# Kernel optimization log

Hardware: AMD Instinct MI355X
Metric: run time of the kernel (lower is better)

The kernel has to match this reference:

```python
import jax, jax.numpy as jnp
import numpy as np

H, KV, D, HID = 32, 8, 128, 4096  # heads, kv heads, head_dim, hidden
BLOCK = 64
SEQLENS = [512, 768, 512, 256]  # packed continuous batch, T = 2048
NUM_BLOCKS = 64


def setup_inputs() -> dict:
    key = jax.random.key(0)
    ks = jax.random.split(key, 8)
    T = int(sum(SEQLENS))
    position_ids = jnp.asarray(np.concatenate([np.arange(l) for l in SEQLENS]), jnp.int64 if False else jnp.int32)
    seq_ids = jnp.asarray(np.concatenate([np.full(l, b) for b, l in enumerate(SEQLENS)]), jnp.int32)
    # assign cache blocks sequentially per sequence, pad rows with 0 (never read)
    max_blocks = max((l + BLOCK - 1) // BLOCK for l in SEQLENS)
    bo = np.zeros((len(SEQLENS), max_blocks), np.int32)
    nxt = 0
    for b, l in enumerate(SEQLENS):
        nb = (l + BLOCK - 1) // BLOCK
        bo[b, :nb] = np.arange(nxt, nxt + nb)
        nxt += nb
    block_offsets = jnp.asarray(bo)
    vision_mask = jax.random.uniform(ks[0], (T,)) < 0.3
    s = 0.02
    return {
        'hidden_states': jax.random.normal(ks[1], (1, T, HID), jnp.float32),
        'position_ids': position_ids,
        'seq_ids': seq_ids,
        'vision_mask': vision_mask,
        'block_offsets': block_offsets,
        'k_cache': jnp.zeros((NUM_BLOCKS, BLOCK, KV, D), jnp.float32),
        'v_cache': jnp.zeros((NUM_BLOCKS, BLOCK, KV, D), jnp.float32),
        'w_qkv_vision': jax.random.normal(ks[2], (HID, HID + 2 * KV * D), jnp.float32) * s,
        'w_qkv_language': jax.random.normal(ks[3], (HID, HID + 2 * KV * D), jnp.float32) * s,
        'w_dense_vision': jax.random.normal(ks[4], (HID, HID), jnp.float32) * s,
        'w_dense_language': jax.random.normal(ks[5], (HID, HID), jnp.float32) * s,
        'inv_freq': 1.0 / (10000.0 ** (jnp.arange(0, D, 2, dtype=jnp.float32) / D)),
    }


def _rope(x, pos, inv_freq):
    # x: [T, h, D]; rotate-half convention as in lmdeploy fused_rotary_emb
    freqs = pos[:, None].astype(jnp.float32) * inv_freq[None, :]  # [T, D/2]
    cos = jnp.cos(freqs)[:, None, :]
    sin = jnp.sin(freqs)[:, None, :]
    x0, x1 = jnp.split(x, 2, axis=-1)
    return jnp.concatenate([x0 * cos - x1 * sin, x1 * cos + x0 * sin], axis=-1)


def reference(hidden_states, position_ids, seq_ids, vision_mask, block_offsets,
              k_cache, v_cache, w_qkv_vision, w_qkv_language,
              w_dense_vision, w_dense_language, inv_freq):
    T = hidden_states.shape[1]
    x = hidden_states[0]  # [T, HID]
    # masked vision/language expert QKV routing
    qkv = jnp.where(vision_mask[:, None], x @ w_qkv_vision, x @ w_qkv_language)
    q, k, v = jnp.split(qkv, [HID, HID + KV * D], axis=-1)
    q = q.reshape(T, H, D)
    k = k.reshape(T, KV, D)
    v = v.reshape(T, KV, D)
    # fused rotary embedding on q, k
    q = _rope(q, position_ids, inv_freq)
    k = _rope(k, position_ids, inv_freq)
    # fill paged KV cache (scatter), then read K/V back through the cache
    blk = block_offsets[seq_ids, position_ids // BLOCK]  # [T]
    slot = position_ids % BLOCK
    k_cache = k_cache.at[blk, slot].set(k)
    v_cache = v_cache.at[blk, slot].set(v)
    k_used = k_cache[blk, slot]  # [T, KV, D]
    v_used = v_cache[blk, slot]
    # GQA paged attention over the packed ragged batch (block-diag causal)
    qg = q.reshape(T, KV, H // KV, D)
    scale = 1.0 / jnp.sqrt(jnp.asarray(D, jnp.float32))
    scores = jnp.einsum('qhgd,khd->hgqk', qg, k_used) * scale  # [KV,G,T,T]
    mask = (seq_ids[:, None] == seq_ids[None, :]) & (position_ids[None, :] <= position_ids[:, None])
    scores = jnp.where(mask[None, None], scores, jnp.asarray(-1e9, scores.dtype))
    probs = jax.nn.softmax(scores, axis=-1)
    ctx = jnp.einsum('hgqk,khd->qhgd', probs, v_used).reshape(T, HID)
    # masked expert dense routing
    attn = jnp.where(vision_mask[:, None], ctx @ w_dense_vision, ctx @ w_dense_language)
    return attn[None], k_cache, v_cache
```

## Files before the change

kernel.cpp:

```cpp
#include <hip/hip_runtime.h>
#include <hip/hip_bf16.h>
#include <stdint.h>

#define T_TOK 2048
#define HID   4096
#define NH    32
#define NKV   8
#define HD    128
#define NQKV  6144
#define QSCALE 0.08838834764831845f

typedef __bf16 bf16x8 __attribute__((ext_vector_type(8)));
typedef float  f32x4  __attribute__((ext_vector_type(4)));
typedef unsigned short su8 __attribute__((ext_vector_type(8)));
typedef unsigned short su4 __attribute__((ext_vector_type(4)));

__device__ __forceinline__ unsigned short f2bf(float f) {
  union { float f; unsigned u; } x; x.f = f;
  unsigned r = x.u + 0x7FFFu + ((x.u >> 16) & 1u);
  return (unsigned short)(r >> 16);
}

__device__ __forceinline__ f32x4 mfma16(su8 a, su8 b, f32x4 c) {
  return __builtin_amdgcn_mfma_f32_16x16x32_bf16(
      __builtin_bit_cast(bf16x8, a), __builtin_bit_cast(bf16x8, b), c, 0, 0, 0);
}

#define GLOAD_LDS16(gp, lp)                                                     \
  __builtin_amdgcn_global_load_lds(                                             \
      (const __attribute__((address_space(1))) void*)(gp),                      \
      (__attribute__((address_space(3))) void*)(lp), 16, 0, 0)

__launch_bounds__(256)
__global__ void route_kernel(const int* __restrict__ vm,
                             int* __restrict__ idx_v, int* __restrict__ idx_l,
                             int* __restrict__ cnts) {
  __shared__ int sv[256], sl[256];
  int tid = threadIdx.x;
  int loc[8]; int lv = 0;
  #pragma unroll
  for (int i = 0; i < 8; i++) { loc[i] = (vm[tid * 8 + i] != 0); lv += loc[i]; }
  int ll = 8 - lv;
  sv[tid] = lv; sl[tid] = ll;
  __syncthreads();
  for (int off = 1; off < 256; off <<= 1) {
    int a = (tid >= off) ? sv[tid - off] : 0;
    int b = (tid >= off) ? sl[tid - off] : 0;
    __syncthreads();
    sv[tid] += a; sl[tid] += b;
    __syncthreads();
  }
  int bv = sv[tid] - lv, bl = sl[tid] - ll;
  #pragma unroll
  for (int i = 0; i < 8; i++) {
    int t = tid * 8 + i;
    if (loc[i]) idx_v[bv++] = t; else idx_l[bl++] = t;
  }
  if (tid == 255) { cnts[0] = sv[255]; cnts[1] = sl[255]; }
}

__launch_bounds__(256)
__global__ void convert_wt(const float* __restrict__ W,
                           unsigned short* __restrict__ Wt, int N) {
  __shared__ float tile[64][65];
  int n0 = blockIdx.x * 64, k0 = blockIdx.y * 64;
  int tid = threadIdx.x;
  int tr = tid >> 4, tc4 = (tid & 15) * 4;
  #pragma unroll
  for (int p = 0; p < 4; p++) {
    int k = p * 16 + tr;
    float4 v = *(const float4*)(W + (size_t)(k0 + k) * N + n0 + tc4);
    tile[tc4 + 0][k] = v.x; tile[tc4 + 1][k] = v.y;
    tile[tc4 + 2][k] = v.z; tile[tc4 + 3][k] = v.w;
  }
  __syncthreads();
  int n = tid >> 2, kc = (tid & 3) * 16;
  unsigned short obuf[16];
  #pragma unroll
  for (int j = 0; j < 16; j++) obuf[j] = f2bf(tile[n][kc + j]);
  su8* dst = (su8*)(Wt + (size_t)(n0 + n) * 4096 + k0 + kc);
  dst[0] = *(su8*)&obuf[0];
  dst[1] = *(su8*)&obuf[8];
}

__launch_bounds__(256)
__global__ void convert_x(const float* __restrict__ x,
                          unsigned short* __restrict__ xb, int n8) {
  int i = blockIdx.x * 256 + threadIdx.x;
  if (i < n8) {
    float4 a = ((const float4*)x)[i * 2], b = ((const float4*)x)[i * 2 + 1];
    su8 u = { f2bf(a.x), f2bf(a.y), f2bf(a.z), f2bf(a.w),
              f2bf(b.x), f2bf(b.y), f2bf(b.z), f2bf(b.w) };
    ((su8*)xb)[i] = u;
  }
}

__launch_bounds__(256)
__global__ void gemm_bf16(const unsigned short* __restrict__ A,
                          const unsigned short* __restrict__ Wv,
                          const unsigned short* __restrict__ Wl,
                          const int* __restrict__ idx_v, const int* __restrict__ idx_l,
                          const int* __restrict__ cnts,
                          float* __restrict__ out, int N) {
  int e = blockIdx.z;
  const unsigned short* Wt = e ? Wl : Wv;
  const int* gidx = e ? idx_l : idx_v;
  int cnt = cnts[e];
  int m0 = blockIdx.y * 128;
  if (m0 >= cnt) return;
  int n0 = blockIdx.x * 128;

  __shared__ __align__(16) unsigned short a_lds[128 * 64];
  __shared__ __align__(16) unsigned short b_lds[128 * 64];

  int tid = threadIdx.x;
  int lane = tid & 63;
  int w = tid >> 6;
  int lg = lane >> 4, lr = lane & 15;
  int wm = w >> 1, wn = w & 1;

  int srow = lane >> 3;
  int scolb = ((lane & 7) ^ srow) << 4;
  const char* a_src[4];
  const char* b_src[4];
  #pragma unroll
  for (int j = 0; j < 4; j++) {
    int c = w * 4 + j;
    int r = c * 8 + srow;
    int gr = gidx[min(m0 + r, cnt - 1)];
    a_src[j] = (const char*)(A + (size_t)gr * 4096) + scolb;
    b_src[j] = (const char*)(Wt + (size_t)(n0 + r) * 4096) + scolb;
  }

  f32x4 acc[4][4];
  #pragma unroll
  for (int fm = 0; fm < 4; fm++)
    #pragma unroll
    for (int fn = 0; fn < 4; fn++)
      acc[fm][fn] = (f32x4){0.f, 0.f, 0.f, 0.f};

  for (int k0 = 0; k0 < 4096; k0 += 64) {
    __syncthreads();
    #pragma unroll
    for (int j = 0; j < 4; j++) {
      int c = w * 4 + j;
      GLOAD_LDS16(a_src[j] + (size_t)k0 * 2, (char*)a_lds + c * 1024);
      GLOAD_LDS16(b_src[j] + (size_t)k0 * 2, (char*)b_lds + c * 1024);
    }
    asm volatile("s_waitcnt vmcnt(0)" ::: "memory");
    __syncthreads();
    #pragma unroll
    for (int s = 0; s < 2; s++) {
      su8 af[4], bfr[4];
      int colb = s * 64 + lg * 16;
      #pragma unroll
      for (int fm = 0; fm < 4; fm++) {
        int r = wm * 64 + fm * 16 + lr;
        af[fm] = *(const su8*)((const char*)a_lds + r * 128 + (colb ^ ((r & 7) << 4)));
      }
      #pragma unroll
      for (int fn = 0; fn < 4; fn++) {
        int r = wn * 64 + fn * 16 + lr;
        bfr[fn] = *(const su8*)((const char*)b_lds + r * 128 + (colb ^ ((r & 7) << 4)));
      }
      #pragma unroll
      for (int fm = 0; fm < 4; fm++)
        #pragma unroll
        for (int fn = 0; fn < 4; fn++)
          acc[fm][fn] = mfma16(af[fm], bfr[fn], acc[fm][fn]);
    }
  }

  #pragma unroll
  for (int fm = 0; fm < 4; fm++) {
    #pragma unroll
    for (int i = 0; i < 4; i++) {
      int r = wm * 64 + fm * 16 + lg * 4 + i;
      if (m0 + r < cnt) {
        int grow = gidx[m0 + r];
        float* orow = out + (size_t)grow * N + n0 + wn * 64;
        #pragma unroll
        for (int fn = 0; fn < 4; fn++)
          orow[fn * 16 + lr] = acc[fm][fn][i];
      }
    }
  }
}

__launch_bounds__(256)
__global__ void gemm_gather(const float* __restrict__ X,
                            const float* __restrict__ Wv, const float* __restrict__ Wl,
                            const int* __restrict__ idx_v, const int* __restrict__ idx_l,
                            const int* __restrict__ cnts,
                            float* __restrict__ out, int N) {
  int e = blockIdx.z;
  const float* W = e ? Wl : Wv;
  const int* gidx = e ? idx_l : idx_v;
  int cnt = cnts[e];
  int m0 = blockIdx.y * 128;
  if (m0 >= cnt) return;
  int n0 = blockIdx.x * 64;

  __shared__ __align__(16) unsigned short a_lds[128][72];
  __shared__ __align__(16) unsigned short b_lds[64][72];

  int tid = threadIdx.x;
  int lane = tid & 63;
  int w = tid >> 6;
  int lg = lane >> 4, lr = lane & 15;
  int wm = w >> 1, wn = w & 1;

  int ar = tid >> 1;
  int akc = (tid & 1) * 32;
  const float* Arow = X + (size_t)gidx[min(m0 + ar, cnt - 1)] * HID;
  int bk = (tid >> 4) * 4;
  int bj = (tid & 15) * 4;

  f32x4 acc[4][2];
  #pragma unroll
  for (int fm = 0; fm < 4; fm++)
    #pragma unroll
    for (int fn = 0; fn < 2; fn++)
      acc[fm][fn] = (f32x4){0.f, 0.f, 0.f, 0.f};

  for (int k0 = 0; k0 < HID; k0 += 64) {
    {
      const float4* src = (const float4*)(Arow + k0 + akc);
      float4 f[8];
      #pragma unroll
      for (int i = 0; i < 8; i++) f[i] = src[i];
      #pragma unroll
      for (int i = 0; i < 4; i++) {
        float4 a0 = f[2 * i], a1 = f[2 * i + 1];
        su8 u = { f2bf(a0.x), f2bf(a0.y), f2bf(a0.z), f2bf(a0.w),
                  f2bf(a1.x), f2bf(a1.y), f2bf(a1.z), f2bf(a1.w) };
        *(su8*)&a_lds[ar][akc + i * 8] = u;
      }
    }
    {
      const float* Wp = W + (size_t)(k0 + bk) * N + n0 + bj;
      float4 r0 = *(const float4*)(Wp);
      float4 r1 = *(const float4*)(Wp + N);
      float4 r2 = *(const float4*)(Wp + 2 * (size_t)N);
      float4 r3 = *(const float4*)(Wp + 3 * (size_t)N);
      su4 c0 = { f2bf(r0.x), f2bf(r1.x), f2bf(r2.x), f2bf(r3.x) };
      su4 c1 = { f2bf(r0.y), f2bf(r1.y), f2bf(r2.y), f2bf(r3.y) };
      su4 c2 = { f2bf(r0.z), f2bf(r1.z), f2bf(r2.z), f2bf(r3.z) };
      su4 c3 = { f2bf(r0.w), f2bf(r1.w), f2bf(r2.w), f2bf(r3.w) };
      *(su4*)&b_lds[bj + 0][bk] = c0;
      *(su4*)&b_lds[bj + 1][bk] = c1;
      *(su4*)&b_lds[bj + 2][bk] = c2;
      *(su4*)&b_lds[bj + 3][bk] = c3;
    }
    __syncthreads();
    #pragma unroll
    for (int s = 0; s < 64; s += 32) {
      su8 af[4], bfr[2];
      #pragma unroll
      for (int fm = 0; fm < 4; fm++)
        af[fm] = *(const su8*)&a_lds[wm * 64 + fm * 16 + lr][s + lg * 8];
      #pragma unroll
      for (int fn = 0; fn < 2; fn++)
        bfr[fn] = *(const su8*)&b_lds[wn * 32 + fn * 16 + lr][s + lg * 8];
      #pragma unroll
      for (int fm = 0; fm < 4; fm++)
        #pragma unroll
        for (int fn = 0; fn < 2; fn++)
          acc[fm][fn] = mfma16(af[fm], bfr[fn], acc[fm][fn]);
    }
    __syncthreads();
  }
  #pragma unroll
  for (int fm = 0; fm < 4; fm++) {
    #pragma unroll
    for (int i = 0; i < 4; i++) {
      int r = wm * 64 + fm * 16 + lg * 4 + i;
      if (m0 + r < cnt) {
        int grow = gidx[m0 + r];
        #pragma unroll
        for (int fn = 0; fn < 2; fn++)
          out[(size_t)grow * N + n0 + wn * 32 + fn * 16 + lr] = acc[fm][fn][i];
      }
    }
  }
}

__launch_bounds__(256)
__global__ void rope_scatter(const float* __restrict__ qkv,
                             const int* __restrict__ pos_ids,
                             const int* __restrict__ seq_ids,
                             const int* __restrict__ block_offsets, int max_blocks,
                             const float* __restrict__ inv_freq,
                             unsigned short* __restrict__ q_ws,
                             unsigned short* __restrict__ k_ws,
                             unsigned short* __restrict__ v_ws,
                             float* __restrict__ kc_out, float* __restrict__ vc_out) {
  int t = blockIdx.x;
  int tid = threadIdx.x;
  __shared__ float cs[64], sn[64];
  int pos = pos_ids[t];
  if (tid < 64) {
    float f = (float)pos * inv_freq[tid];
    float s, c;
    sincosf(f, &s, &c);
    cs[tid] = c; sn[tid] = s;
  }
  __syncthreads();
  const float* row = qkv + (size_t)t * NQKV;
  #pragma unroll 4
  for (int it = 0; it < 16; it++) {
    int idx = it * 256 + tid;
    int hh = idx >> 7, d = idx & 127;
    float val;
    if (d < 64) val = row[hh * 128 + d] * cs[d] - row[hh * 128 + d + 64] * sn[d];
    else { int j = d - 64; val = row[hh * 128 + d] * cs[j] + row[hh * 128 + j] * sn[j]; }
    q_ws[((size_t)hh * T_TOK + t) * HD + d] = f2bf(val * QSCALE);
  }
  int seq = seq_ids[t];
  int blk = block_offsets[seq * max_blocks + (pos >> 6)];
  int slot = pos & 63;
  #pragma unroll
  for (int it = 0; it < 4; it++) {
    int idx = it * 256 + tid;
    int kvh = idx >> 7, d = idx & 127;
    const float* kr = row + HID;
    float val;
    if (d < 64) val = kr[kvh * 128 + d] * cs[d] - kr[kvh * 128 + d + 64] * sn[d];
    else { int j = d - 64; val = kr[kvh * 128 + d] * cs[j] + kr[kvh * 128 + j] * sn[j]; }
    kc_out[(((size_t)blk * 64 + slot) * NKV + kvh) * HD + d] = val;
    k_ws[((size_t)kvh * T_TOK + t) * HD + d] = f2bf(val);
  }
  #pragma unroll
  for (int it = 0; it < 4; it++) {
    int idx = it * 256 + tid;
    int kvh = idx >> 7, d = idx & 127;
    float val = row[HID + NKV * HD + idx];
    vc_out[(((size_t)blk * 64 + slot) * NKV + kvh) * HD + d] = val;
    v_ws[((size_t)kvh * T_TOK + t) * HD + d] = f2bf(val);
  }
}

template <bool BF16OUT>
__launch_bounds__(256)
__global__ void attn_kernel(const unsigned short* __restrict__ q_ws,
                            const unsigned short* __restrict__ k_ws,
                            const unsigned short* __restrict__ v_ws,
                            const int* __restrict__ pos_ids,
                            void* __restrict__ ctx) {
  int qt = blockIdx.x;
  int h = blockIdx.y;
  int kvh = h >> 2;
  int t0 = qt * 64;

  __shared__ __align__(16) unsigned short q_lds[64][136];
  __shared__ __align__(16) unsigned short k_lds[64][136];
  __shared__ __align__(16) unsigned short v_lds[128][72];
  __shared__ __align__(16) unsigned short p_lds[4][16][72];

  int tid = threadIdx.x;
  int lane = tid & 63;
  int w = tid >> 6;
  int lg = lane >> 4, lr = lane & 15;

  int seq_start = t0 - pos_ids[t0];
  int nkb = (t0 - seq_start) / 64 + 1;

  {
    int r = tid >> 2, dc = (tid & 3) * 32;
    const su8* src = (const su8*)(q_ws + ((size_t)h * T_TOK + t0 + r) * HD + dc);
    #pragma unroll
    for (int i = 0; i < 4; i++) *(su8*)&q_lds[r][dc + i * 8] = src[i];
  }
  __syncthreads();
  su8 qf[4];
  #pragma unroll
  for (int s = 0; s < 4; s++)
    qf[s] = *(const su8*)&q_lds[w * 16 + lr][s * 32 + lg * 8];

  f32x4 O[8];
  #pragma unroll
  for (int fd = 0; fd < 8; fd++) O[fd] = (f32x4){0.f, 0.f, 0.f, 0.f};
  float m_i[4] = { -1e30f, -1e30f, -1e30f, -1e30f };
  float l_i[4] = { 0.f, 0.f, 0.f, 0.f };

  for (int kb = 0; kb < nkb; kb++) {
    int kt0 = seq_start + kb * 64;
    __syncthreads();
    {
      int r = tid >> 2, dc = (tid & 3) * 32;
      const su8* src = (const su8*)(k_ws + ((size_t)kvh * T_TOK + kt0 + r) * HD + dc);
      #pragma unroll
      for (int i = 0; i < 4; i++) *(su8*)&k_lds[r][dc + i * 8] = src[i];
    }
    {
      int d0 = (tid & 31) * 4, key0 = (tid >> 5) * 8;
      su4 vv[8];
      #pragma unroll
      for (int r = 0; r < 8; r++)
        vv[r] = *(const su4*)(v_ws + ((size_t)kvh * T_TOK + kt0 + key0 + r) * HD + d0);
      #pragma unroll
      for (int dd = 0; dd < 4; dd++) {
        su8 u = { vv[0][dd], vv[1][dd], vv[2][dd], vv[3][dd],
                  vv[4][dd], vv[5][dd], vv[6][dd], vv[7][dd] };
        *(su8*)&v_lds[d0 + dd][key0] = u;
      }
    }
    __syncthreads();

    f32x4 S[4];
    #pragma unroll
    for (int f = 0; f < 4; f++) S[f] = (f32x4){0.f, 0.f, 0.f, 0.f};
    #pragma unroll
    for (int f = 0; f < 4; f++) {
      #pragma unroll
      for (int s = 0; s < 4; s++) {
        su8 kf = *(const su8*)&k_lds[f * 16 + lr][s * 32 + lg * 8];
        S[f] = mfma16(qf[s], kf, S[f]);
      }
    }
    if (kt0 == t0) {
      #pragma unroll
      for (int f = 0; f < 4; f++)
        #pragma unroll
        for (int i = 0; i < 4; i++)
          if (f * 16 + lr > w * 16 + lg * 4 + i) S[f][i] = -1e30f;
    }
    float mnew[4], alpha[4];
    #pragma unroll
    for (int i = 0; i < 4; i++) {
      float mx = fmaxf(fmaxf(S[0][i], S[1][i]), fmaxf(S[2][i], S[3][i]));
      #pragma unroll
      for (int off = 8; off > 0; off >>= 1) mx = fmaxf(mx, __shfl_xor(mx, off, 16));
      mnew[i] = fmaxf(m_i[i], mx);
      alpha[i] = __expf(m_i[i] - mnew[i]);
      m_i[i] = mnew[i];
    }
    float rs[4] = { 0.f, 0.f, 0.f, 0.f };
    #pragma unroll
    for (int f = 0; f < 4; f++)
      #pragma unroll
      for (int i = 0; i < 4; i++) {
        float p = __expf(S[f][i] - mnew[i]);
        S[f][i] = p;
        rs[i] += p;
      }
    #pragma unroll
    for (int i = 0; i < 4; i++) {
      #pragma unroll
      for (int off = 8; off > 0; off >>= 1) rs[i] += __shfl_xor(rs[i], off, 16);
      l_i[i] = l_i[i] * alpha[i] + rs[i];
    }
    #pragma unroll
    for (int f = 0; f < 4; f++)
      #pragma unroll
      for (int i = 0; i < 4; i++)
        p_lds[w][lg * 4 + i][f * 16 + lr] = f2bf(S[f][i]);
    #pragma unroll
    for (int fd = 0; fd < 8; fd++)
      #pragma unroll
      for (int i = 0; i < 4; i++)
        O[fd][i] *= alpha[i];
    #pragma unroll
    for (int kk = 0; kk < 2; kk++) {
      su8 pf = *(const su8*)&p_lds[w][lr][kk * 32 + lg * 8];
      #pragma unroll
      for (int fd = 0; fd < 8; fd++) {
        su8 vf = *(const su8*)&v_lds[fd * 16 + lr][kk * 32 + lg * 8];
        O[fd] = mfma16(pf, vf, O[fd]);
      }
    }
  }

  #pragma unroll
  for (int i = 0; i < 4; i++) {
    float inv = 1.f / l_i[i];
    int tq = t0 + w * 16 + lg * 4 + i;
    #pragma unroll
    for (int fd = 0; fd < 8; fd++) {
      size_t off = (size_t)tq * HID + h * HD + fd * 16 + lr;
      if (BF16OUT) ((unsigned short*)ctx)[off] = f2bf(O[fd][i] * inv);
      else ((float*)ctx)[off] = O[fd][i] * inv;
    }
  }
}

extern "C" void kernel_launch(void* const* d_in, const int* in_sizes, int n_in,
                              void* d_out, int out_size, void* d_ws, size_t ws_size,
                              hipStream_t stream) {
  const float* hidden = (const float*)d_in[0];
  const int* pos = (const int*)d_in[1];
  const int* seq = (const int*)d_in[2];
  const int* vmask = (const int*)d_in[3];
  const int* bo = (const int*)d_in[4];
  const float* kc_in = (const float*)d_in[5];
  const float* vc_in = (const float*)d_in[6];
  const float* wqv = (const float*)d_in[7];
  const float* wql = (const float*)d_in[8];
  const float* wdv = (const float*)d_in[9];
  const float* wdl = (const float*)d_in[10];
  const float* invf = (const float*)d_in[11];
  int max_blocks = in_sizes[4] / 4;

  float* out_attn = (float*)d_out;
  float* kc_out = out_attn + (size_t)T_TOK * HID;
  float* vc_out = kc_out + (size_t)4194304;

  (void)hipMemcpyAsync(kc_out, kc_in, (size_t)4194304 * 4, hipMemcpyDeviceToDevice, stream);
  (void)hipMemcpyAsync(vc_out, vc_in, (size_t)4194304 * 4, hipMemcpyDeviceToDevice, stream);

  char* ws = (char*)d_ws;
  const size_t WT_BYTES   = 100663296;
  const size_t R0_BYTES   = 67108864;
  const size_t REQ = WT_BYTES + R0_BYTES + 16777216  + 2 * 4194304  + 32768;

  if (ws_size >= REQ) {
    unsigned short* wt0   = (unsigned short*)ws;
    unsigned short* wt_qv = wt0;
    unsigned short* wt_ql = wt0 + (size_t)25165824;
    unsigned short* wt_dv = wt0;
    unsigned short* wt_dl = wt0 + (size_t)16777216;
    float* qkv_f32        = (float*)(ws + WT_BYTES);
    unsigned short* ctx_bf = (unsigned short*)(ws + WT_BYTES);
    unsigned short* x_bf  = (unsigned short*)(ws + WT_BYTES + 50331648);
    unsigned short* q_ws  = (unsigned short*)(ws + WT_BYTES + R0_BYTES);
    unsigned short* k_ws  = q_ws + (size_t)NH * T_TOK * HD;
    unsigned short* v_ws  = k_ws + (size_t)NKV * T_TOK * HD;
    int* idx_v = (int*)(v_ws + (size_t)NKV * T_TOK * HD);
    int* idx_l = idx_v + T_TOK;
    int* cnts  = idx_l + T_TOK;

    route_kernel<<<1, 256, 0, stream>>>(vmask, idx_v, idx_l, cnts);
    convert_wt<<<dim3(96, 64), 256, 0, stream>>>(wqv, wt_qv, NQKV);
    convert_wt<<<dim3(96, 64), 256, 0, stream>>>(wql, wt_ql, NQKV);
    convert_x<<<4096, 256, 0, stream>>>(hidden, x_bf, T_TOK * HID / 8);
    gemm_bf16<<<dim3(NQKV / 128, 16, 2), 256, 0, stream>>>(
        x_bf, wt_qv, wt_ql, idx_v, idx_l, cnts, qkv_f32, NQKV);
    rope_scatter<<<T_TOK, 256, 0, stream>>>(
        qkv_f32, pos, seq, bo, max_blocks, invf, q_ws, k_ws, v_ws, kc_out, vc_out);
    convert_wt<<<dim3(64, 64), 256, 0, stream>>>(wdv, wt_dv, HID);
    convert_wt<<<dim3(64, 64), 256, 0, stream>>>(wdl, wt_dl, HID);
    attn_kernel<true><<<dim3(T_TOK / 64, NH), 256, 0, stream>>>(
        q_ws, k_ws, v_ws, pos, (void*)ctx_bf);
    gemm_bf16<<<dim3(HID / 128, 16, 2), 256, 0, stream>>>(
        ctx_bf, wt_dv, wt_dl, idx_v, idx_l, cnts, out_attn, HID);
  } else {
    float* qkv_ws = (float*)ws;
    float* ctx_ws = (float*)ws;
    size_t off = (size_t)T_TOK * NQKV * 4;
    unsigned short* q_ws = (unsigned short*)(ws + off);
    unsigned short* k_ws = q_ws + (size_t)NH * T_TOK * HD;
    unsigned short* v_ws = k_ws + (size_t)NKV * T_TOK * HD;
    int* idx_v = (int*)(v_ws + (size_t)NKV * T_TOK * HD);
    int* idx_l = idx_v + T_TOK;
    int* cnts = idx_l + T_TOK;

    route_kernel<<<1, 256, 0, stream>>>(vmask, idx_v, idx_l, cnts);
    gemm_gather<<<dim3(NQKV / 64, 16, 2), 256, 0, stream>>>(
        hidden, wqv, wql, idx_v, idx_l, cnts, qkv_ws, NQKV);
    rope_scatter<<<T_TOK, 256, 0, stream>>>(
        qkv_ws, pos, seq, bo, max_blocks, invf, q_ws, k_ws, v_ws, kc_out, vc_out);
    attn_kernel<false><<<dim3(T_TOK / 64, NH), 256, 0, stream>>>(
        q_ws, k_ws, v_ws, pos, (void*)ctx_ws);
    gemm_gather<<<dim3(HID / 64, 16, 2), 256, 0, stream>>>(
        ctx_ws, wdv, wdl, idx_v, idx_l, cnts, out_attn, HID);
  }
}
```

Measured before the change: 516.3 us.

## Double-buffer LDS in bf16 GEMM and merge paired weight conversion launches

The bf16 GEMM main loop now keeps two LDS buffers. It issues global-to-LDS loads for the next K slice before running the MFMAs on the current one, so memory latency can overlap with compute instead of being serialized behind a full wait and barrier. Separately, each pair of vision/language weight conversions is merged into a single launch using blockIdx.z, which removes launch overhead and gives each launch more blocks. LDS use per block doubles to 64KB, which may lower occupancy, and the single barrier per stage has to be enough to protect the buffer being overwritten.

```diff
diff --git a/kernel.cpp b/kernel.cpp
--- a/kernel.cpp
+++ b/kernel.cpp
@@ -60,8 +60,11 @@
 }
 
 __launch_bounds__(256)
-__global__ void convert_wt(const float* __restrict__ W,
-                           unsigned short* __restrict__ Wt, int N) {
+__global__ void convert_wt2(const float* __restrict__ W0, const float* __restrict__ W1,
+                            unsigned short* __restrict__ Wt0, unsigned short* __restrict__ Wt1,
+                            int N) {
+  const float* W = blockIdx.z ? W1 : W0;
+  unsigned short* Wt = blockIdx.z ? Wt1 : Wt0;
   __shared__ float tile[64][65];
   int n0 = blockIdx.x * 64, k0 = blockIdx.y * 64;
   int tid = threadIdx.x;
@@ -110,8 +113,8 @@
   if (m0 >= cnt) return;
   int n0 = blockIdx.x * 128;
 
-  __shared__ __align__(16) unsigned short a_lds[128 * 64];
-  __shared__ __align__(16) unsigned short b_lds[128 * 64];
+  __shared__ __align__(16) unsigned short a_lds[2][128 * 64];
+  __shared__ __align__(16) unsigned short b_lds[2][128 * 64];
 
   int tid = threadIdx.x;
   int lane = tid & 63;
@@ -139,16 +142,15 @@
     for (int fn = 0; fn < 4; fn++)
       acc[fm][fn] = (f32x4){0.f, 0.f, 0.f, 0.f};
 
-  for (int k0 = 0; k0 < 4096; k0 += 64) {
-    __syncthreads();
+  auto STAGE = [&](unsigned short* la, unsigned short* lb, size_t kb) {
     #pragma unroll
     for (int j = 0; j < 4; j++) {
       int c = w * 4 + j;
-      GLOAD_LDS16(a_src[j] + (size_t)k0 * 2, (char*)a_lds + c * 1024);
-      GLOAD_LDS16(b_src[j] + (size_t)k0 * 2, (char*)b_lds + c * 1024);
-    }
-    asm volatile("s_waitcnt vmcnt(0)" ::: "memory");
-    __syncthreads();
+      GLOAD_LDS16(a_src[j] + kb, (char*)la + c * 1024);
+      GLOAD_LDS16(b_src[j] + kb, (char*)lb + c * 1024);
+    }
+  };
+  auto COMPUTE = [&](const unsigned short* la, const unsigned short* lb) {
     #pragma unroll
     for (int s = 0; s < 2; s++) {
       su8 af[4], bfr[4];
@@ -156,12 +158,12 @@
       #pragma unroll
       for (int fm = 0; fm < 4; fm++) {
         int r = wm * 64 + fm * 16 + lr;
-        af[fm] = *(const su8*)((const char*)a_lds + r * 128 + (colb ^ ((r & 7) << 4)));
+        af[fm] = *(const su8*)((const char*)la + r * 128 + (colb ^ ((r & 7) << 4)));
       }
       #pragma unroll
       for (int fn = 0; fn < 4; fn++) {
         int r = wn * 64 + fn * 16 + lr;
-        bfr[fn] = *(const su8*)((const char*)b_lds + r * 128 + (colb ^ ((r & 7) << 4)));
+        bfr[fn] = *(const su8*)((const char*)lb + r * 128 + (colb ^ ((r & 7) << 4)));
       }
       #pragma unroll
       for (int fm = 0; fm < 4; fm++)
@@ -169,6 +171,21 @@
         for (int fn = 0; fn < 4; fn++)
           acc[fm][fn] = mfma16(af[fm], bfr[fn], acc[fm][fn]);
     }
+  };
+
+  STAGE(a_lds[0], b_lds[0], 0);
+  asm volatile("s_waitcnt vmcnt(0)" ::: "memory");
+  __builtin_amdgcn_s_barrier();
+
+  for (int k0 = 0; k0 < 4096; k0 += 128) {
+    if (k0 + 64 < 4096) STAGE(a_lds[1], b_lds[1], (size_t)(k0 + 64) * 2);
+    COMPUTE(a_lds[0], b_lds[0]);
+    asm volatile("s_waitcnt vmcnt(0)" ::: "memory");
+    __builtin_amdgcn_s_barrier();
+    if (k0 + 128 < 4096) STAGE(a_lds[0], b_lds[0], (size_t)(k0 + 128) * 2);
+    COMPUTE(a_lds[1], b_lds[1]);
+    asm volatile("s_waitcnt vmcnt(0)" ::: "memory");
+    __builtin_amdgcn_s_barrier();
   }
 
   #pragma unroll
@@ -530,15 +547,13 @@
     int* cnts  = idx_l + T_TOK;
 
     route_kernel<<<1, 256, 0, stream>>>(vmask, idx_v, idx_l, cnts);
-    convert_wt<<<dim3(96, 64), 256, 0, stream>>>(wqv, wt_qv, NQKV);
-    convert_wt<<<dim3(96, 64), 256, 0, stream>>>(wql, wt_ql, NQKV);
+    convert_wt2<<<dim3(96, 64, 2), 256, 0, stream>>>(wqv, wql, wt_qv, wt_ql, NQKV);
     convert_x<<<4096, 256, 0, stream>>>(hidden, x_bf, T_TOK * HID / 8);
     gemm_bf16<<<dim3(NQKV / 128, 16, 2), 256, 0, stream>>>(
         x_bf, wt_qv, wt_ql, idx_v, idx_l, cnts, qkv_f32, NQKV);
     rope_scatter<<<T_TOK, 256, 0, stream>>>(
         qkv_f32, pos, seq, bo, max_blocks, invf, q_ws, k_ws, v_ws, kc_out, vc_out);
-    convert_wt<<<dim3(64, 64), 256, 0, stream>>>(wdv, wt_dv, HID);
-    convert_wt<<<dim3(64, 64), 256, 0, stream>>>(wdl, wt_dl, HID);
+    convert_wt2<<<dim3(64, 64, 2), 256, 0, stream>>>(wdv, wdl, wt_dv, wt_dl, HID);
     attn_kernel<true><<<dim3(T_TOK / 64, NH), 256, 0, stream>>>(
         q_ws, k_ws, v_ws, pos, (void*)ctx_bf);
     gemm_bf16<<<dim3(HID / 128, 16, 2), 256, 0, stream>>>(
```

Measured after the change: 537.6 us. 1.04x slower.
